# Kernel optimization log

Measured on AMD Instinct MI355X. Metric: run time of the kernel, lower is better.

The kernel has to match this reference:

```python
import jax, jax.numpy as jnp
import numpy as np

B, N, D, H = 128, 128, 1024, 8
HD = D // H  # 128; NOTE: N must equal HD due to the module's einsum pattern
SCALE = HD ** -0.5


def _split_heads(x):
    # [b, n, h*d] -> [b, h, n, d]
    b, n, _ = x.shape
    return x.reshape(b, n, H, HD).transpose(0, 2, 1, 3)


def setup_inputs() -> dict:
    key = jax.random.key(0)
    ks = jax.random.split(key, 12)
    s = D ** -0.5
    return {
        "words": jax.random.normal(ks[0], (B, N, D), jnp.float32),
        "position": jax.random.normal(ks[1], (B, N, D), jnp.float32),
        "conscious": jax.random.normal(ks[2], (B, N, D), jnp.float32),
        "Wq_w": jax.random.normal(ks[3], (D, D), jnp.float32) * s,
        "Wk_w": jax.random.normal(ks[4], (D, D), jnp.float32) * s,
        "Wv_w": jax.random.normal(ks[5], (D, D), jnp.float32) * s,
        "Wq_p": jax.random.normal(ks[6], (D, D), jnp.float32) * s,
        "Wk_p": jax.random.normal(ks[7], (D, D), jnp.float32) * s,
        "Wq_c": jax.random.normal(ks[8], (D, D), jnp.float32) * s,
        "Wk_c": jax.random.normal(ks[9], (D, D), jnp.float32) * s,
        "Wo": jax.random.normal(ks[10], (D, D), jnp.float32) * s,
        "bo": jax.random.normal(ks[11], (D,), jnp.float32) * 0.01,
    }


def reference(words, position, conscious, Wq_w, Wk_w, Wv_w, Wq_p, Wk_p, Wq_c, Wk_c, Wo, bo):
    q_w = _split_heads(words @ Wq_w)
    k_w = _split_heads(words @ Wk_w)
    v_w = _split_heads(words @ Wv_w)
    q_p = _split_heads(position @ Wq_p)
    k_p = _split_heads(position @ Wk_p)
    q_c = _split_heads(conscious @ Wq_c)
    k_c = _split_heads(conscious @ Wk_c)

    # Faithful to source: 'b h i j, b h j d -> b h i d' contracts q's head dim
    # with k's seq dim (requires N == HD). Three score streams summed.
    sim = (jnp.einsum('bhij,bhjd->bhid', q_w, k_w)
           + jnp.einsum('bhij,bhjd->bhid', q_p, k_p)
           + jnp.einsum('bhij,bhjd->bhid', q_c, k_c)) * SCALE
    attn = jax.nn.softmax(sim, axis=-1)
    out = jnp.einsum('bhij,bhjd->bhid', attn, v_w)  # [b,h,n,d]
    out = out.transpose(0, 2, 1, 3).reshape(B, N, D)  # merge heads
    return out @ Wo + bo
```

## Files before the change

kernel.cpp:

```cpp
#include <hip/hip_runtime.h>


typedef unsigned short u16;
typedef __attribute__((ext_vector_type(8))) short bf16x8;
typedef __attribute__((ext_vector_type(4))) short bf16x4;
typedef __attribute__((ext_vector_type(4))) float f32x4;

__device__ __forceinline__ float bf2f(u16 x) {
  union { unsigned u; float f; } v;
  v.u = ((unsigned)x) << 16;
  return v.f;
}

__device__ __forceinline__ u16 f2bf(float f) {
  union { float f; unsigned u; } v;
  v.f = f;
  unsigned r = v.u + 0x7fffu + ((v.u >> 16) & 1u);
  return (u16)(r >> 16);
}

__device__ __forceinline__ float ldv(const void* p, size_t i, int f32) {
  return f32 ? ((const float*)p)[i] : bf2f(((const u16*)p)[i]);
}

__device__ __forceinline__ f32x4 MFMA(bf16x8 a, bf16x8 b, f32x4 c) {
  return __builtin_amdgcn_mfma_f32_16x16x32_bf16(a, b, c, 0, 0, 0);
}

#define GLDS16(gp, lp)                                               \
  __builtin_amdgcn_global_load_lds(                                  \
      (const __attribute__((address_space(1))) unsigned int*)(gp),   \
      (__attribute__((address_space(3))) unsigned int*)(lp), 16, 0, 0)

__device__ __forceinline__ bf16x8 lds_frag(const u16* ls, int row, int cb) {
  const int byte = (row * 128 + cb) ^ ((row & 7) << 4);
  return *(const bf16x8*)((const char*)ls + byte);
}

__global__ void detect_dtype(const void* words, int* flag) {
  __shared__ int cnt;
  if (threadIdx.x == 0) cnt = 0;
  __syncthreads();
  const u16* w = (const u16*)words;
  int local = 0;
  for (int i = threadIdx.x; i < 2048; i += 256) {
    const u16 v = w[2 * i];
    const int e = (v >> 7) & 0xFF;
    if (v == 0 || (e >= 0x60 && e <= 0x8F)) local++;
  }
  atomicAdd(&cnt, local);
  __syncthreads();
  if (threadIdx.x == 0) *flag = (cnt >= 1434) ? 0 : 1;
}

__global__ __launch_bounds__(256) void cast_w(
    const void* w0, const void* w1, const void* w2, const void* w3,
    const void* w4, const void* w5, const void* w6, const void* w7,
    u16* __restrict__ WT, const int* __restrict__ flag) {
  __shared__ float t[32][33];
  const int f32 = *flag;
  const int p = blockIdx.z;
  const void* W;
  switch (p) {
    case 0: W = w0; break; case 1: W = w1; break; case 2: W = w2; break;
    case 3: W = w3; break; case 4: W = w4; break; case 5: W = w5; break;
    case 6: W = w6; break; default: W = w7; break;
  }
  const int k0 = blockIdx.y * 32, n0 = blockIdx.x * 32;
  const int tx = threadIdx.x & 31, ry = threadIdx.x >> 5;
  for (int r = ry; r < 32; r += 8)
    t[r][tx] = ldv(W, (size_t)(k0 + r) * 1024 + n0 + tx, f32);
  __syncthreads();
  u16* dst = WT + (size_t)p * 1048576ull;
  for (int r = ry; r < 32; r += 8)
    dst[(size_t)(n0 + r) * 1024 + k0 + tx] = f2bf(t[tx][r]);
}

__global__ __launch_bounds__(256) void cast_a(
    const void* x0, const void* x1, const void* x2, u16* __restrict__ Abf,
    int b0, int chb, const int* __restrict__ flag) {
  const int f32 = *flag;
  const int t = blockIdx.z;
  const void* src = (t == 0) ? x0 : ((t == 1) ? x1 : x2);
  u16* dst = Abf + (size_t)t * (size_t)chb * 131072ull;
  const size_t n4 = (size_t)chb * 32768ull;
  const size_t off = (size_t)b0 * 131072ull;
  const size_t stride = (size_t)gridDim.x * 256ull;
  if (f32) {
    const float4* s = (const float4*)src + off / 4;
    for (size_t i = (size_t)blockIdx.x * 256 + threadIdx.x; i < n4; i += stride) {
      const float4 v = s[i];
      bf16x4 o = { (short)f2bf(v.x), (short)f2bf(v.y),
                   (short)f2bf(v.z), (short)f2bf(v.w) };
      *(bf16x4*)&dst[i * 4] = o;
    }
  } else {
    const bf16x4* s = (const bf16x4*)((const u16*)src + off);
    for (size_t i = (size_t)blockIdx.x * 256 + threadIdx.x; i < n4; i += stride)
      ((bf16x4*)dst)[i] = s[i];
  }
}

__global__ __launch_bounds__(256) void proj_mfma(
    const u16* __restrict__ Abf, const u16* __restrict__ WT,
    u16* __restrict__ P, int chb) {
  __shared__ u16 lsA[128 * 64];
  __shared__ u16 lsB[128 * 64];
  const int p = blockIdx.z;
  const int asel = (p < 3) ? 0 : ((p < 5) ? 1 : 2);
  const u16* A = Abf + (size_t)asel * (size_t)chb * 131072ull;
  const u16* W = WT + (size_t)p * 1048576ull;
  u16* C = P + (size_t)p * (size_t)chb * 131072ull;
  const int tr = (p == 1) | (p == 2) | (p == 4) | (p == 6);

  int wg = blockIdx.y * 8 + blockIdx.x;
  const int nwg = (int)gridDim.y * 8;
  wg = (wg & 7) * (nwg >> 3) + (wg >> 3);
  const int bx = wg & 7, by = wg >> 3;

  const int tn = bx * 128;
  const int tm = by * 128;
  const int w = threadIdx.x >> 6, l = threadIdx.x & 63;
  const int wm = w >> 1, wn = w & 1;
  const int lr = l >> 3;
  const int lc = ((l & 7) * 16) ^ (lr << 4);
  const int fr = l & 15, fq = l >> 4;

  f32x4 acc[4][4] = {};
  for (int kt = 0; kt < 1024; kt += 64) {
    #pragma unroll
    for (int c = 0; c < 4; ++c) {
      GLDS16(&A[(size_t)(tm + w * 32 + c * 8 + lr) * 1024 + kt + (lc >> 1)],
             &lsA[(w * 32 + c * 8) * 64]);
      GLDS16(&W[(size_t)(tn + w * 32 + c * 8 + lr) * 1024 + kt + (lc >> 1)],
             &lsB[(w * 32 + c * 8) * 64]);
    }
    __syncthreads();
    #pragma unroll
    for (int ks = 0; ks < 2; ++ks) {
      bf16x8 af[4], bfr[4];
      const int cb = ks * 64 + fq * 16;
      #pragma unroll
      for (int m = 0; m < 4; ++m)
        af[m] = lds_frag(lsA, wm * 64 + m * 16 + fr, cb);
      #pragma unroll
      for (int n = 0; n < 4; ++n)
        bfr[n] = lds_frag(lsB, wn * 64 + n * 16 + fr, cb);
      #pragma unroll
      for (int m = 0; m < 4; ++m)
        #pragma unroll
        for (int n = 0; n < 4; ++n)
          acc[m][n] = MFMA(af[m], bfr[n], acc[m][n]);
    }
    __syncthreads();
  }

  if (!tr) {
    #pragma unroll
    for (int m = 0; m < 4; ++m)
      #pragma unroll
      for (int n = 0; n < 4; ++n)
        #pragma unroll
        for (int r = 0; r < 4; ++r) {
          const int row = tm + wm * 64 + m * 16 + fq * 4 + r;
          const int col = tn + wn * 64 + n * 16 + fr;
          C[(size_t)row * 1024 + col] = f2bf(acc[m][n][r]);
        }
  } else {
    const size_t tb = ((size_t)by * 8 + bx) * 16384ull;
    #pragma unroll
    for (int m = 0; m < 4; ++m)
      #pragma unroll
      for (int n = 0; n < 4; ++n) {
        const int d = wn * 64 + n * 16 + fr;
        const int j0 = wm * 64 + m * 16 + fq * 4;
        bf16x4 v = { (short)f2bf(acc[m][n][0]), (short)f2bf(acc[m][n][1]),
                     (short)f2bf(acc[m][n][2]), (short)f2bf(acc[m][n][3]) };
        *(bf16x4*)&C[tb + (size_t)d * 128 + j0] = v;
      }
  }
}

__global__ __launch_bounds__(256) void attn_mfma(
    const u16* __restrict__ P, int chb, u16* __restrict__ merged) {
  __shared__ u16 pl[16384];
  const int h = blockIdx.x, b = blockIdx.y;
  const int w = threadIdx.x >> 6, l = threadIdx.x & 63;
  const size_t MS = (size_t)chb * 131072ull;
  const u16* const Qs[3] = { P, P + 3 * MS, P + 5 * MS };
  const u16* const Ks[3] = { P + 1 * MS, P + 4 * MS, P + 6 * MS };
  const u16* V = P + 2 * MS;
  const size_t qb = (size_t)b * 131072ull + (size_t)h * 128;
  const size_t kb = ((size_t)b * 8 + h) * 16384ull;

  f32x4 acc[2][8] = {};
  #pragma unroll
  for (int kt = 0; kt < 128; kt += 32) {
    #pragma unroll
    for (int t = 0; t < 3; ++t) {
      bf16x8 a[2];
      #pragma unroll
      for (int m = 0; m < 2; ++m)
        a[m] = *(const bf16x8*)&Qs[t][qb + (size_t)(w * 32 + m * 16 + (l & 15)) * 1024
                                       + kt + (l >> 4) * 8];
      #pragma unroll
      for (int n = 0; n < 8; ++n) {
        const bf16x8 bb = *(const bf16x8*)&Ks[t][kb + (size_t)(n * 16 + (l & 15)) * 128
                                                 + kt + (l >> 4) * 8];
        acc[0][n] = MFMA(a[0], bb, acc[0][n]);
        acc[1][n] = MFMA(a[1], bb, acc[1][n]);
      }
    }
  }

  const float SC = 0.08838834764831845f;
  #pragma unroll
  for (int m = 0; m < 2; ++m)
    #pragma unroll
    for (int r = 0; r < 4; ++r) {
      float mx = -3.0e38f;
      #pragma unroll
      for (int n = 0; n < 8; ++n) {
        acc[m][n][r] *= SC;
        mx = fmaxf(mx, acc[m][n][r]);
      }
      #pragma unroll
      for (int s = 1; s < 16; s <<= 1) mx = fmaxf(mx, __shfl_xor(mx, s));
      float sm = 0.f;
      #pragma unroll
      for (int n = 0; n < 8; ++n) {
        const float e = __expf(acc[m][n][r] - mx);
        acc[m][n][r] = e;
        sm += e;
      }
      #pragma unroll
      for (int s = 1; s < 16; s <<= 1) sm += __shfl_xor(sm, s);
      const float inv = 1.f / sm;
      #pragma unroll
      for (int n = 0; n < 8; ++n) acc[m][n][r] *= inv;
    }

  #pragma unroll
  for (int m = 0; m < 2; ++m)
    #pragma unroll
    for (int n = 0; n < 8; ++n)
      #pragma unroll
      for (int r = 0; r < 4; ++r) {
        const int row = w * 32 + m * 16 + (l >> 4) * 4 + r;
        const int col = n * 16 + (l & 15);
        const int byte = (row * 256 + col * 2) ^ ((row & 7) << 4);
        *(u16*)((char*)pl + byte) = f2bf(acc[m][n][r]);
      }
  __syncthreads();

  f32x4 o[2][8] = {};
  #pragma unroll
  for (int kt = 0; kt < 128; kt += 32) {
    bf16x8 a[2];
    #pragma unroll
    for (int m = 0; m < 2; ++m) {
      const int row = w * 32 + m * 16 + (l & 15);
      const int byte = (row * 256 + (kt + (l >> 4) * 8) * 2) ^ ((row & 7) << 4);
      a[m] = *(const bf16x8*)((char*)pl + byte);
    }
    #pragma unroll
    for (int n = 0; n < 8; ++n) {
      const bf16x8 bb = *(const bf16x8*)&V[kb + (size_t)(n * 16 + (l & 15)) * 128
                                           + kt + (l >> 4) * 8];
      o[0][n] = MFMA(a[0], bb, o[0][n]);
      o[1][n] = MFMA(a[1], bb, o[1][n]);
    }
  }

  #pragma unroll
  for (int m = 0; m < 2; ++m)
    #pragma unroll
    for (int n = 0; n < 8; ++n)
      #pragma unroll
      for (int r = 0; r < 4; ++r) {
        const int row = w * 32 + m * 16 + (l >> 4) * 4 + r;
        const int col = n * 16 + (l & 15);
        merged[(size_t)(b * 128 + row) * 1024 + h * 128 + col] = f2bf(o[m][n][r]);
      }
}

__global__ __launch_bounds__(256) void final_mfma(
    const u16* __restrict__ A, const u16* __restrict__ W,
    const void* __restrict__ bias, void* __restrict__ out, int b0,
    const int* __restrict__ flag) {
  __shared__ u16 lsA[128 * 64];
  __shared__ u16 lsB[128 * 64];
  const int f32 = *flag;

  int wg = blockIdx.y * 8 + blockIdx.x;
  const int nwg = (int)gridDim.y * 8;
  wg = (wg & 7) * (nwg >> 3) + (wg >> 3);
  const int bx = wg & 7, by = wg >> 3;

  const int tn = bx * 128;
  const int tm = by * 128;
  const int w = threadIdx.x >> 6, l = threadIdx.x & 63;
  const int wm = w >> 1, wn = w & 1;
  const int lr = l >> 3;
  const int lc = ((l & 7) * 16) ^ (lr << 4);
  const int fr = l & 15, fq = l >> 4;

  f32x4 acc[4][4] = {};
  for (int kt = 0; kt < 1024; kt += 64) {
    #pragma unroll
    for (int c = 0; c < 4; ++c) {
      GLDS16(&A[(size_t)(tm + w * 32 + c * 8 + lr) * 1024 + kt + (lc >> 1)],
             &lsA[(w * 32 + c * 8) * 64]);
      GLDS16(&W[(size_t)(tn + w * 32 + c * 8 + lr) * 1024 + kt + (lc >> 1)],
             &lsB[(w * 32 + c * 8) * 64]);
    }
    __syncthreads();
    #pragma unroll
    for (int ks = 0; ks < 2; ++ks) {
      bf16x8 af[4], bfr[4];
      const int cb = ks * 64 + fq * 16;
      #pragma unroll
      for (int m = 0; m < 4; ++m)
        af[m] = lds_frag(lsA, wm * 64 + m * 16 + fr, cb);
      #pragma unroll
      for (int n = 0; n < 4; ++n)
        bfr[n] = lds_frag(lsB, wn * 64 + n * 16 + fr, cb);
      #pragma unroll
      for (int m = 0; m < 4; ++m)
        #pragma unroll
        for (int n = 0; n < 4; ++n)
          acc[m][n] = MFMA(af[m], bfr[n], acc[m][n]);
    }
    __syncthreads();
  }

  #pragma unroll
  for (int m = 0; m < 4; ++m)
    #pragma unroll
    for (int n = 0; n < 4; ++n)
      #pragma unroll
      for (int r = 0; r < 4; ++r) {
        const int row = tm + wm * 64 + m * 16 + fq * 4 + r;
        const int col = tn + wn * 64 + n * 16 + fr;
        const float rv = acc[m][n][r] + ldv(bias, col, f32);
        const size_t g = (size_t)(b0 * 128 + row) * 1024 + col;
        if (f32) ((float*)out)[g] = rv;
        else ((u16*)out)[g] = f2bf(rv);
      }
}

extern "C" void kernel_launch(void* const* d_in, const int* in_sizes, int n_in,
                              void* d_out, int out_size, void* d_ws, size_t ws_size,
                              hipStream_t stream) {
  const size_t fixed = 64ull + 8ull * 1048576ull * 2ull;
  int CHB = 128;
  while (CHB > 1 && fixed + 11ull * (size_t)CHB * 131072ull * 2ull > ws_size)
    CHB >>= 1;

  int* flag = (int*)d_ws;
  u16* WT = (u16*)((char*)d_ws + 64);
  u16* Abf = WT + 8ull * 1048576ull;
  u16* P = Abf + 3ull * (size_t)CHB * 131072ull;
  u16* merged = P + 7ull * (size_t)CHB * 131072ull;

  detect_dtype<<<1, 256, 0, stream>>>(d_in[0], flag);
  cast_w<<<dim3(32, 32, 8), 256, 0, stream>>>(
      d_in[3], d_in[4], d_in[5], d_in[6], d_in[7], d_in[8], d_in[9], d_in[10],
      WT, flag);

  for (int b0 = 0; b0 < 128; b0 += CHB) {
    cast_a<<<dim3(512, 1, 3), 256, 0, stream>>>(
        d_in[0], d_in[1], d_in[2], Abf, b0, CHB, flag);
    proj_mfma<<<dim3(8, CHB, 7), 256, 0, stream>>>(Abf, WT, P, CHB);
    attn_mfma<<<dim3(8, CHB), 256, 0, stream>>>(P, CHB, merged);
    final_mfma<<<dim3(8, CHB), 256, 0, stream>>>(
        merged, WT + 7ull * 1048576ull, d_in[11], d_out, b0, flag);
  }
}
```

Before: 834.8 us.

## Enlarge projection GEMM tiles to 256x256 with double-buffered LDS pipelining

The projection GEMM moves from 128x128 tiles with 256 threads to 256x256 tiles with 512 threads. Global-to-LDS loads are double-buffered so the next K slice is prefetched while MFMAs run, with explicit waitcnt, barriers and setprio. The workspace is also trimmed by aliasing the merged buffer onto the cast-input buffer, which allows larger batch chunks. This costs 64KB of LDS and more registers per block, and the transposed-store index math is generalised to handle tiles spanning two batches or heads.

Result: slower. 876.5 us (+5.0%).

```diff
diff --git a/kernel.cpp b/kernel.cpp
--- a/kernel.cpp
+++ b/kernel.cpp
@@ -101,11 +101,11 @@
   }
 }
 
-__global__ __launch_bounds__(256) void proj_mfma(
+__global__ __launch_bounds__(512, 2) void proj_mfma(
     const u16* __restrict__ Abf, const u16* __restrict__ WT,
     u16* __restrict__ P, int chb) {
-  __shared__ u16 lsA[128 * 64];
-  __shared__ u16 lsB[128 * 64];
+  __shared__ u16 lsA[2][2][8192];
+  __shared__ u16 lsB[2][2][8192];
   const int p = blockIdx.z;
   const int asel = (p < 3) ? 0 : ((p < 5) ? 1 : 2);
   const u16* A = Abf + (size_t)asel * (size_t)chb * 131072ull;
@@ -113,69 +113,99 @@
   u16* C = P + (size_t)p * (size_t)chb * 131072ull;
   const int tr = (p == 1) | (p == 2) | (p == 4) | (p == 6);
 
-  int wg = blockIdx.y * 8 + blockIdx.x;
-  const int nwg = (int)gridDim.y * 8;
-  wg = (wg & 7) * (nwg >> 3) + (wg >> 3);
-  const int bx = wg & 7, by = wg >> 3;
-
-  const int tn = bx * 128;
-  const int tm = by * 128;
+  int wg = blockIdx.y * 4 + blockIdx.x;
+  const int nwg = (int)gridDim.y * 4;
+  if (!(nwg & 7)) wg = (wg & 7) * (nwg >> 3) + (wg >> 3);
+  const int bx = wg & 3, by = wg >> 2;
+  const int tn = bx * 256, tm = by * 256;
+
   const int w = threadIdx.x >> 6, l = threadIdx.x & 63;
-  const int wm = w >> 1, wn = w & 1;
+  const int wm = w >> 2, wn = w & 3;
   const int lr = l >> 3;
-  const int lc = ((l & 7) * 16) ^ (lr << 4);
+  const int lgr = (l & 7) ^ lr;
   const int fr = l & 15, fq = l >> 4;
-
-  f32x4 acc[4][4] = {};
-  for (int kt = 0; kt < 1024; kt += 64) {
-    #pragma unroll
-    for (int c = 0; c < 4; ++c) {
-      GLDS16(&A[(size_t)(tm + w * 32 + c * 8 + lr) * 1024 + kt + (lc >> 1)],
-             &lsA[(w * 32 + c * 8) * 64]);
-      GLDS16(&W[(size_t)(tn + w * 32 + c * 8 + lr) * 1024 + kt + (lc >> 1)],
-             &lsB[(w * 32 + c * 8) * 64]);
-    }
-    __syncthreads();
-    #pragma unroll
-    for (int ks = 0; ks < 2; ++ks) {
+  const int srow0 = w * 16;
+
+#define STAGE(kt, s)                                                      \
+  {                                                                       \
+    const int k0 = (kt) * 64 + lgr * 8;                                   \
+    _Pragma("unroll")                                                     \
+    for (int c = 0; c < 2; ++c) {                                         \
+      const int rr = srow0 + c * 8 + lr;                                  \
+      GLDS16(&A[(size_t)(tm + rr) * 1024 + k0],                           \
+             &lsA[s][0][(srow0 + c * 8) * 64]);                           \
+      GLDS16(&A[(size_t)(tm + 128 + rr) * 1024 + k0],                     \
+             &lsA[s][1][(srow0 + c * 8) * 64]);                           \
+      GLDS16(&W[(size_t)(tn + rr) * 1024 + k0],                           \
+             &lsB[s][0][(srow0 + c * 8) * 64]);                           \
+      GLDS16(&W[(size_t)(tn + 128 + rr) * 1024 + k0],                     \
+             &lsB[s][1][(srow0 + c * 8) * 64]);                           \
+    }                                                                     \
+  }
+
+  f32x4 acc[8][4] = {};
+
+  STAGE(0, 0);
+  STAGE(1, 1);
+  asm volatile("s_waitcnt vmcnt(8)" ::: "memory");
+  __builtin_amdgcn_s_barrier();
+
+  #pragma unroll 2
+  for (int t = 0; t < 16; ++t) {
+    const int s = t & 1;
+    #pragma unroll
+    for (int q = 0; q < 4; ++q) {
+      const int mh = q & 1, ks = q >> 1;
+      const int cb = ks * 64 + fq * 16;
       bf16x8 af[4], bfr[4];
-      const int cb = ks * 64 + fq * 16;
       #pragma unroll
       for (int m = 0; m < 4; ++m)
-        af[m] = lds_frag(lsA, wm * 64 + m * 16 + fr, cb);
+        af[m] = lds_frag(&lsA[s][wm][0], mh * 64 + m * 16 + fr, cb);
       #pragma unroll
       for (int n = 0; n < 4; ++n)
-        bfr[n] = lds_frag(lsB, wn * 64 + n * 16 + fr, cb);
+        bfr[n] = lds_frag(&lsB[s][wn >> 1][0], (wn & 1) * 64 + n * 16 + fr, cb);
+      if (q == 3 && t < 14) STAGE(t + 2, s);
+      __builtin_amdgcn_s_barrier();
+      asm volatile("s_waitcnt lgkmcnt(0)" ::: "memory");
+      __builtin_amdgcn_s_setprio(1);
       #pragma unroll
       for (int m = 0; m < 4; ++m)
         #pragma unroll
         for (int n = 0; n < 4; ++n)
-          acc[m][n] = MFMA(af[m], bfr[n], acc[m][n]);
-    }
-    __syncthreads();
-  }
+          acc[mh * 4 + m][n] = MFMA(af[m], bfr[n], acc[mh * 4 + m][n]);
+      __builtin_amdgcn_s_setprio(0);
+      if (q == 3) {
+        if (t < 14) asm volatile("s_waitcnt vmcnt(8)" ::: "memory");
+        else        asm volatile("s_waitcnt vmcnt(0)" ::: "memory");
+      }
+      __builtin_amdgcn_s_barrier();
+    }
+  }
+#undef STAGE
 
   if (!tr) {
     #pragma unroll
-    for (int m = 0; m < 4; ++m)
-      #pragma unroll
-      for (int n = 0; n < 4; ++n)
+    for (int im = 0; im < 8; ++im)
+      #pragma unroll
+      for (int n = 0; n < 4; ++n) {
+        const int row = tm + wm * 128 + (im >> 2) * 64 + (im & 3) * 16 + fq * 4;
+        const int col = tn + wn * 64 + n * 16 + fr;
         #pragma unroll
-        for (int r = 0; r < 4; ++r) {
-          const int row = tm + wm * 64 + m * 16 + fq * 4 + r;
-          const int col = tn + wn * 64 + n * 16 + fr;
-          C[(size_t)row * 1024 + col] = f2bf(acc[m][n][r]);
-        }
+        for (int r = 0; r < 4; ++r)
+          C[(size_t)(row + r) * 1024 + col] = f2bf(acc[im][n][r]);
+      }
   } else {
-    const size_t tb = ((size_t)by * 8 + bx) * 16384ull;
-    #pragma unroll
-    for (int m = 0; m < 4; ++m)
+    #pragma unroll
+    for (int im = 0; im < 8; ++im)
       #pragma unroll
       for (int n = 0; n < 4; ++n) {
-        const int d = wn * 64 + n * 16 + fr;
-        const int j0 = wm * 64 + m * 16 + fq * 4;
-        bf16x4 v = { (short)f2bf(acc[m][n][0]), (short)f2bf(acc[m][n][1]),
-                     (short)f2bf(acc[m][n][2]), (short)f2bf(acc[m][n][3]) };
+        const int grow = tm + wm * 128 + (im >> 2) * 64 + (im & 3) * 16 + fq * 4;
+        const int gcol = tn + wn * 64 + n * 16 + fr;
+        const int b = grow >> 7, j0 = grow & 127;
+        const int h = gcol >> 7, d = gcol & 127;
+        const size_t tb = ((size_t)b * 8 + h) * 16384ull;
+        bf16x4 v = { (short)f2bf(acc[im][n][0]), (short)f2bf(acc[im][n][1]),
+                     (short)f2bf(acc[im][n][2]), (short)f2bf(acc[im][n][3]) };
         *(bf16x4*)&C[tb + (size_t)d * 128 + j0] = v;
       }
   }
@@ -354,14 +384,14 @@
                               hipStream_t stream) {
   const size_t fixed = 64ull + 8ull * 1048576ull * 2ull;
   int CHB = 128;
-  while (CHB > 1 && fixed + 11ull * (size_t)CHB * 131072ull * 2ull > ws_size)
+  while (CHB > 2 && fixed + 10ull * (size_t)CHB * 131072ull * 2ull > ws_size)
     CHB >>= 1;
 
   int* flag = (int*)d_ws;
   u16* WT = (u16*)((char*)d_ws + 64);
   u16* Abf = WT + 8ull * 1048576ull;
   u16* P = Abf + 3ull * (size_t)CHB * 131072ull;
-  u16* merged = P + 7ull * (size_t)CHB * 131072ull;
+  u16* merged = Abf;
 
   detect_dtype<<<1, 256, 0, stream>>>(d_in[0], flag);
   cast_w<<<dim3(32, 32, 8), 256, 0, stream>>>(
@@ -371,7 +401,7 @@
   for (int b0 = 0; b0 < 128; b0 += CHB) {
     cast_a<<<dim3(512, 1, 3), 256, 0, stream>>>(
         d_in[0], d_in[1], d_in[2], Abf, b0, CHB, flag);
-    proj_mfma<<<dim3(8, CHB, 7), 256, 0, stream>>>(Abf, WT, P, CHB);
+    proj_mfma<<<dim3(4, CHB / 2, 7), 512, 0, stream>>>(Abf, WT, P, CHB);
     attn_mfma<<<dim3(8, CHB), 256, 0, stream>>>(P, CHB, merged);
     final_mfma<<<dim3(8, CHB), 256, 0, stream>>>(
         merged, WT + 7ull * 1048576ull, d_in[11], d_out, b0, flag);
```

## Stage GEMM and attention epilogues through LDS for coalesced 16-byte stores

Applied to the files above, without the earlier changes.

The proj, attention and final kernels now write accumulator fragments into swizzled shared memory first. They then read them back as whole rows and emit 16-byte (or float4) global stores instead of scattered 2-byte or 8-byte stores. The merged buffer now aliases the activation cast buffer, which lowers the workspace need and may allow larger batch chunks. The cost is extra LDS traffic and barriers in each epilogue, and the final kernel runs its staging in two halves.

Result: faster. 729.3 us (-12.6%).

```diff
diff --git a/kernel.cpp b/kernel.cpp
--- a/kernel.cpp
+++ b/kernel.cpp
@@ -35,6 +35,10 @@
 __device__ __forceinline__ bf16x8 lds_frag(const u16* ls, int row, int cb) {
   const int byte = (row * 128 + cb) ^ ((row & 7) << 4);
   return *(const bf16x8*)((const char*)ls + byte);
+}
+
+__device__ __forceinline__ int cs_byte(int row, int colb) {
+  return (row * 256 + colb) ^ ((row & 7) << 4);
 }
 
 __global__ void detect_dtype(const void* words, int* flag) {
@@ -104,8 +108,9 @@
 __global__ __launch_bounds__(256) void proj_mfma(
     const u16* __restrict__ Abf, const u16* __restrict__ WT,
     u16* __restrict__ P, int chb) {
-  __shared__ u16 lsA[128 * 64];
-  __shared__ u16 lsB[128 * 64];
+  __shared__ u16 lds[16384];
+  u16* lsA = lds;
+  u16* lsB = lds + 8192;
   const int p = blockIdx.z;
   const int asel = (p < 3) ? 0 : ((p < 5) ? 1 : 2);
   const u16* A = Abf + (size_t)asel * (size_t)chb * 131072ull;
@@ -155,29 +160,36 @@
     __syncthreads();
   }
 
+  #pragma unroll
+  for (int m = 0; m < 4; ++m)
+    #pragma unroll
+    for (int n = 0; n < 4; ++n)
+      #pragma unroll
+      for (int r = 0; r < 4; ++r) {
+        const int row = wm * 64 + m * 16 + fq * 4 + r;
+        const int col = wn * 64 + n * 16 + fr;
+        const int sr = tr ? col : row;
+        const int sc = tr ? row : col;
+        *(u16*)((char*)lds + cs_byte(sr, sc * 2)) = f2bf(acc[m][n][r]);
+      }
+  __syncthreads();
+  const int crow = threadIdx.x >> 4;
+  const int ccb = (threadIdx.x & 15) * 16;
   if (!tr) {
     #pragma unroll
-    for (int m = 0; m < 4; ++m)
-      #pragma unroll
-      for (int n = 0; n < 4; ++n)
-        #pragma unroll
-        for (int r = 0; r < 4; ++r) {
-          const int row = tm + wm * 64 + m * 16 + fq * 4 + r;
-          const int col = tn + wn * 64 + n * 16 + fr;
-          C[(size_t)row * 1024 + col] = f2bf(acc[m][n][r]);
-        }
+    for (int pass = 0; pass < 8; ++pass) {
+      const int row = pass * 16 + crow;
+      const bf16x8 v = *(const bf16x8*)((const char*)lds + cs_byte(row, ccb));
+      *(bf16x8*)&C[(size_t)(tm + row) * 1024 + tn + (ccb >> 1)] = v;
+    }
   } else {
     const size_t tb = ((size_t)by * 8 + bx) * 16384ull;
     #pragma unroll
-    for (int m = 0; m < 4; ++m)
-      #pragma unroll
-      for (int n = 0; n < 4; ++n) {
-        const int d = wn * 64 + n * 16 + fr;
-        const int j0 = wm * 64 + m * 16 + fq * 4;
-        bf16x4 v = { (short)f2bf(acc[m][n][0]), (short)f2bf(acc[m][n][1]),
-                     (short)f2bf(acc[m][n][2]), (short)f2bf(acc[m][n][3]) };
-        *(bf16x4*)&C[tb + (size_t)d * 128 + j0] = v;
-      }
+    for (int pass = 0; pass < 8; ++pass) {
+      const int d = pass * 16 + crow;
+      const bf16x8 v = *(const bf16x8*)((const char*)lds + cs_byte(d, ccb));
+      *(bf16x8*)&C[tb + (size_t)d * 128 + (ccb >> 1)] = v;
+    }
   }
 }
 
@@ -272,6 +284,7 @@
     }
   }
 
+  __syncthreads();
   #pragma unroll
   for (int m = 0; m < 2; ++m)
     #pragma unroll
@@ -280,16 +293,26 @@
       for (int r = 0; r < 4; ++r) {
         const int row = w * 32 + m * 16 + (l >> 4) * 4 + r;
         const int col = n * 16 + (l & 15);
-        merged[(size_t)(b * 128 + row) * 1024 + h * 128 + col] = f2bf(o[m][n][r]);
-      }
+        *(u16*)((char*)pl + cs_byte(row, col * 2)) = f2bf(o[m][n][r]);
+      }
+  __syncthreads();
+  const int crow = threadIdx.x >> 4;
+  const int ccb = (threadIdx.x & 15) * 16;
+  #pragma unroll
+  for (int pass = 0; pass < 8; ++pass) {
+    const int row = pass * 16 + crow;
+    const bf16x8 v = *(const bf16x8*)((const char*)pl + cs_byte(row, ccb));
+    *(bf16x8*)&merged[(size_t)(b * 128 + row) * 1024 + h * 128 + (ccb >> 1)] = v;
+  }
 }
 
 __global__ __launch_bounds__(256) void final_mfma(
     const u16* __restrict__ A, const u16* __restrict__ W,
     const void* __restrict__ bias, void* __restrict__ out, int b0,
     const int* __restrict__ flag) {
-  __shared__ u16 lsA[128 * 64];
-  __shared__ u16 lsB[128 * 64];
+  __shared__ u16 lds[16384];
+  u16* lsA = lds;
+  u16* lsB = lds + 8192;
   const int f32 = *flag;
 
   int wg = blockIdx.y * 8 + blockIdx.x;
@@ -334,19 +357,44 @@
     __syncthreads();
   }
 
-  #pragma unroll
-  for (int m = 0; m < 4; ++m)
-    #pragma unroll
-    for (int n = 0; n < 4; ++n)
-      #pragma unroll
-      for (int r = 0; r < 4; ++r) {
-        const int row = tm + wm * 64 + m * 16 + fq * 4 + r;
-        const int col = tn + wn * 64 + n * 16 + fr;
-        const float rv = acc[m][n][r] + ldv(bias, col, f32);
-        const size_t g = (size_t)(b0 * 128 + row) * 1024 + col;
-        if (f32) ((float*)out)[g] = rv;
-        else ((u16*)out)[g] = f2bf(rv);
-      }
+  float* fs = (float*)lds;
+  const int crow = threadIdx.x >> 4;
+  const int cq = threadIdx.x & 15;
+  #pragma unroll
+  for (int half = 0; half < 2; ++half) {
+    #pragma unroll
+    for (int n2 = 0; n2 < 2; ++n2) {
+      const int n = half * 2 + n2;
+      #pragma unroll
+      for (int m = 0; m < 4; ++m)
+        #pragma unroll
+        for (int r = 0; r < 4; ++r) {
+          const int row = wm * 64 + m * 16 + fq * 4 + r;
+          const int cpos = wn * 32 + n2 * 16 + fr;
+          const int col = tn + wn * 64 + n * 16 + fr;
+          const int byte = (row * 256 + cpos * 4) ^ ((row & 7) << 4);
+          *(float*)((char*)fs + byte) = acc[m][n][r] + ldv(bias, col, f32);
+        }
+    }
+    __syncthreads();
+    #pragma unroll
+    for (int pass = 0; pass < 8; ++pass) {
+      const int row = pass * 16 + crow;
+      const int byte = (row * 256 + cq * 16) ^ ((row & 7) << 4);
+      const float4 v = *(const float4*)((const char*)fs + byte);
+      const int cpos = cq * 4;
+      const int gcol = tn + (cpos >> 5) * 64 + half * 32 + (cpos & 31);
+      const size_t g = (size_t)(b0 * 128 + tm + row) * 1024 + gcol;
+      if (f32) {
+        *(float4*)&((float*)out)[g] = v;
+      } else {
+        bf16x4 o = { (short)f2bf(v.x), (short)f2bf(v.y),
+                     (short)f2bf(v.z), (short)f2bf(v.w) };
+        *(bf16x4*)&((u16*)out)[g] = o;
+      }
+    }
+    __syncthreads();
+  }
 }
 
 extern "C" void kernel_launch(void* const* d_in, const int* in_sizes, int n_in,
@@ -354,14 +402,14 @@
                               hipStream_t stream) {
   const size_t fixed = 64ull + 8ull * 1048576ull * 2ull;
   int CHB = 128;
-  while (CHB > 1 && fixed + 11ull * (size_t)CHB * 131072ull * 2ull > ws_size)
+  while (CHB > 2 && fixed + 10ull * (size_t)CHB * 131072ull * 2ull > ws_size)
     CHB >>= 1;
 
   int* flag = (int*)d_ws;
   u16* WT = (u16*)((char*)d_ws + 64);
   u16* Abf = WT + 8ull * 1048576ull;
   u16* P = Abf + 3ull * (size_t)CHB * 131072ull;
-  u16* merged = P + 7ull * (size_t)CHB * 131072ull;
+  u16* merged = Abf;
 
   detect_dtype<<<1, 256, 0, stream>>>(d_in[0], flag);
   cast_w<<<dim3(32, 32, 8), 256, 0, stream>>>(
```
